# Kernel tuning notes

Measured on AMD Instinct MI355X. Metric: run time of the kernel, lower is better.

Reference implementation:

```python
import jax, jax.numpy as jnp
import numpy as np

N_HEADS = 16
ROPE_DIMS = 64


def _rope_tables(T, rd):
    # freqs: 1 / 10000^(arange(0, rd, 2)/rd), shape [rd//2]
    freqs = 1.0 / (10000.0 ** (np.arange(0, rd, 2, dtype=np.float32) / np.float32(rd)))
    ang = np.outer(np.arange(T, dtype=np.float32), freqs)  # [T, rd//2]
    return jnp.asarray(np.cos(ang)), jnp.asarray(np.sin(ang))


def _apply_rope(x, cos, sin, rd):
    # x: [B, H, T, D]; rotate-half style on first rd dims
    x_rope, x_pass = x[..., :rd], x[..., rd:]
    x1, x2 = x_rope[..., : rd // 2], x_rope[..., rd // 2 :]
    c = cos[None, None]  # [1,1,T,rd//2]
    s = sin[None, None]
    x_rot = jnp.concatenate([x1 * c - x2 * s, x2 * c + x1 * s], axis=-1)
    return jnp.concatenate([x_rot, x_pass], axis=-1)


def setup_inputs() -> dict:
    key = jax.random.key(0)
    k1, k2, k3 = jax.random.split(key, 3)
    B, T, C = 32, 512, 2048
    x = jax.random.normal(k1, (B, T, C), dtype=jnp.float32)
    w_qkv = jax.random.normal(k2, (3 * C, C), dtype=jnp.float32) * 0.02
    w_out = jax.random.normal(k3, (C, C), dtype=jnp.float32) * 0.02
    return {"x": x, "w_qkv": w_qkv, "w_out": w_out}


def reference(x, w_qkv, w_out):
    B, T, C = x.shape
    H = N_HEADS
    D = C // H
    # fused QKV projection: F.linear(x, w) = x @ w.T
    qkv = jnp.einsum('btc,fc->btf', x, w_qkv).reshape(B, T, 3, H, D)
    q = jnp.transpose(qkv[:, :, 0], (0, 2, 1, 3))  # [B,H,T,D]
    k = jnp.transpose(qkv[:, :, 1], (0, 2, 1, 3))
    v = jnp.transpose(qkv[:, :, 2], (0, 2, 1, 3))
    cos, sin = _rope_tables(T, ROPE_DIMS)
    q = _apply_rope(q, cos, sin, ROPE_DIMS)
    k = _apply_rope(k, cos, sin, ROPE_DIMS)
    # causal SDPA
    scale = 1.0 / jnp.sqrt(jnp.asarray(D, dtype=x.dtype))
    scores = jnp.einsum('bhqd,bhkd->bhqk', q, k) * scale
    causal = jnp.tril(jnp.ones((T, T), dtype=bool))
    scores = jnp.where(causal[None, None], scores, jnp.finfo(scores.dtype).min)
    attn = jax.nn.softmax(scores, axis=-1)
    y = jnp.einsum('bhqk,bhkd->bhqd', attn, v)
    y = jnp.transpose(y, (0, 2, 1, 3)).reshape(B, T, C)
    return jnp.einsum('btc,fc->btf', y, w_out)
```

## Files before the change

### kernel.cpp

```cpp
#include <hip/hip_runtime.h>


typedef __bf16 bf16x8 __attribute__((ext_vector_type(8)));
typedef float floatx4 __attribute__((ext_vector_type(4)));

__device__ __forceinline__ unsigned short f2bf(float f) {
  union { float f; unsigned u; } v; v.f = f;
  unsigned r = v.u + 0x7FFFu + ((v.u >> 16) & 1u);
  return (unsigned short)(r >> 16);
}
__device__ __forceinline__ float bf2f(unsigned short h) {
  union { unsigned u; float f; } v; v.u = ((unsigned)h) << 16; return v.f;
}

__device__ __forceinline__ void load_lds16(const void* g, void* l) {
  __builtin_amdgcn_global_load_lds((__attribute__((address_space(1))) void*)g,
                                   (__attribute__((address_space(3))) void*)l,
                                   16, 0, 0);
}

#define BARRIER() asm volatile("s_barrier" ::: "memory")
#define VMCNT6()  asm volatile("s_waitcnt vmcnt(6)" ::: "memory")
#define VMCNT0()  asm volatile("s_waitcnt vmcnt(0)" ::: "memory")

__global__ void rope_tables(float* __restrict__ cost, float* __restrict__ sint) {
  int i = blockIdx.x * 256 + threadIdx.x;
  if (i >= 512 * 32) return;
  int t = i >> 5, f = i & 31;
  float e = -(float)(2 * f) / 64.0f;
  float freq = powf(10000.0f, e);
  float ang = (float)t * freq;
  cost[i] = cosf(ang);
  sint[i] = sinf(ang);
}

__global__ void cast_bf16(const float* __restrict__ in,
                          unsigned short* __restrict__ out, int n8) {
  int i = blockIdx.x * 256 + threadIdx.x;
  if (i >= n8) return;
  float4 a = ((const float4*)in)[2 * i];
  float4 b = ((const float4*)in)[2 * i + 1];
  union { uint4 v; unsigned short u[8]; } o;
  o.u[0] = f2bf(a.x); o.u[1] = f2bf(a.y); o.u[2] = f2bf(a.z); o.u[3] = f2bf(a.w);
  o.u[4] = f2bf(b.x); o.u[5] = f2bf(b.y); o.u[6] = f2bf(b.z); o.u[7] = f2bf(b.w);
  ((uint4*)out)[i] = o.v;
}

__global__ __launch_bounds__(256) void rope_apply(
    unsigned short* __restrict__ qkv, const float* __restrict__ cost,
    const float* __restrict__ sint) {
  const int idx = blockIdx.x * 256 + threadIdx.x;
  const int tok = idx >> 4, h = idx & 15;
  const int t = tok & 511;
  const float scale = 0.08838834764831845f * 1.4426950408889634f;
  unsigned short* qrow = qkv + (size_t)tok * 6144 + h * 128;
  unsigned short* krow = qrow + 2048;

  float cs[32], sn[32];
#pragma unroll
  for (int j = 0; j < 8; ++j) {
    *(float4*)&cs[j * 4] = *(const float4*)&cost[t * 32 + j * 4];
    *(float4*)&sn[j * 4] = *(const float4*)&sint[t * 32 + j * 4];
  }
  union u32x4 { uint4 v[4]; unsigned short u[32]; };
  u32x4 q1, q2, k1, k2, o1, o2, o3, o4;
#pragma unroll
  for (int j = 0; j < 4; ++j) {
    q1.v[j] = *(const uint4*)(qrow + j * 8);
    q2.v[j] = *(const uint4*)(qrow + 32 + j * 8);
    k1.v[j] = *(const uint4*)(krow + j * 8);
    k2.v[j] = *(const uint4*)(krow + 32 + j * 8);
  }
#pragma unroll
  for (int d = 0; d < 32; ++d) {
    float c = cs[d], s = sn[d];
    float qx1 = bf2f(q1.u[d]), qx2 = bf2f(q2.u[d]);
    o1.u[d] = f2bf((qx1 * c - qx2 * s) * scale);
    o2.u[d] = f2bf((qx2 * c + qx1 * s) * scale);
    float kx1 = bf2f(k1.u[d]), kx2 = bf2f(k2.u[d]);
    o3.u[d] = f2bf(kx1 * c - kx2 * s);
    o4.u[d] = f2bf(kx2 * c + kx1 * s);
  }
#pragma unroll
  for (int j = 0; j < 4; ++j) {
    *(uint4*)(qrow + j * 8)      = o1.v[j];
    *(uint4*)(qrow + 32 + j * 8) = o2.v[j];
    *(uint4*)(krow + j * 8)      = o3.v[j];
    *(uint4*)(krow + 32 + j * 8) = o4.v[j];
  }
#pragma unroll
  for (int j = 0; j < 8; ++j) {
    union { uint4 v; unsigned short u[8]; } p, po;
    p.v = *(const uint4*)(qrow + 64 + j * 8);
#pragma unroll
    for (int jj = 0; jj < 8; ++jj) po.u[jj] = f2bf(bf2f(p.u[jj]) * scale);
    *(uint4*)(qrow + 64 + j * 8) = po.v;
  }
}

template <int OUT_BF16>
__global__ __launch_bounds__(512, 2) void gemm256(
    const unsigned short* __restrict__ A, const unsigned short* __restrict__ Bt,
    void* __restrict__ Cout, int M, int N, int K) {
  __shared__ __align__(16) unsigned short As[2][16384];
  __shared__ __align__(16) unsigned short Bs[2][16384];

  const int tid = threadIdx.x;
  const int nbx = gridDim.x;
  const int nwg = nbx * gridDim.y;
  const int lin = blockIdx.y * nbx + blockIdx.x;
  const int swz = (lin & 7) * (nwg >> 3) + (lin >> 3);
  const int bm = swz / nbx, bn = swz % nbx;

  const int w = tid >> 6, l = tid & 63;
  const int wm = w >> 2, wn = w & 3;
  const int quad = l >> 4, cl = l & 15;
  const int xs0 = ((0 + quad) ^ (cl & 7)) << 3;
  const int xs1 = ((4 + quad) ^ (cl & 7)) << 3;
  const int aoff = (wm * 128 + cl) * 64;
  const int boff = (wn * 64 + cl) * 64;

  const int srow = tid >> 3;
  const int lc = (tid & 7) ^ (srow & 7);
  const unsigned short* Ag = A + (size_t)(bm * 256 + srow) * K + lc * 8;
  const unsigned short* Bg = Bt + (size_t)(bn * 256 + srow) * K + lc * 8;

  auto stageA = [&](int q, int h, int k0) {
    const unsigned short* src = Ag + (size_t)(h * 128) * K + k0;
    unsigned short* dst = &As[q][0] + h * 8192 + tid * 8;
    load_lds16(src, dst);
    load_lds16(src + (size_t)64 * K, dst + 4096);
  };
  auto stageB = [&](int q, int h, int k0) {
    const unsigned short* src = Bg + (size_t)(h * 128) * K + k0;
    unsigned short* dst = &Bs[q][0] + h * 8192 + tid * 8;
    load_lds16(src, dst);
    load_lds16(src + (size_t)64 * K, dst + 4096);
  };

  floatx4 acc[8][4] = {};
  const int NT = K >> 6;

  stageA(0, 0, 0);  stageA(0, 1, 0);  stageB(0, 0, 0);  stageB(0, 1, 0);
  stageA(1, 0, 64); stageA(1, 1, 64); stageB(1, 0, 64);
  VMCNT6();
  BARRIER();

  for (int t = 0; t < NT; ++t) {
    const int q = t & 1;
    const unsigned short* pA = &As[q][0] + aoff;
    const unsigned short* pB = &Bs[q][0] + boff;
    const int k2 = (t + 2) << 6;
    const bool s2 = (t + 2) < NT;

    bf16x8 a0[4][2], a1[4][2], b0[2][2], b1[2][2];
#pragma unroll
    for (int mi = 0; mi < 4; ++mi) {
      a0[mi][0] = *(const bf16x8*)(pA + mi * 1024 + xs0);
      a0[mi][1] = *(const bf16x8*)(pA + mi * 1024 + xs1);
    }
#pragma unroll
    for (int ni = 0; ni < 2; ++ni) {
      b0[ni][0] = *(const bf16x8*)(pB + ni * 1024 + xs0);
      b0[ni][1] = *(const bf16x8*)(pB + ni * 1024 + xs1);
    }
    if (t + 1 < NT) stageB(q ^ 1, 1, (t + 1) << 6);
    BARRIER();
    __builtin_amdgcn_s_setprio(1);
#pragma unroll
    for (int mi = 0; mi < 4; ++mi)
#pragma unroll
      for (int ni = 0; ni < 2; ++ni)
#pragma unroll
        for (int ks = 0; ks < 2; ++ks)
          acc[mi][ni] = __builtin_amdgcn_mfma_f32_16x16x32_bf16(
              a0[mi][ks], b0[ni][ks], acc[mi][ni], 0, 0, 0);
    __builtin_amdgcn_s_setprio(0);
    BARRIER();
#pragma unroll
    for (int mi = 0; mi < 4; ++mi) {
      a1[mi][0] = *(const bf16x8*)(pA + (mi + 4) * 1024 + xs0);
      a1[mi][1] = *(const bf16x8*)(pA + (mi + 4) * 1024 + xs1);
    }
    BARRIER();
    __builtin_amdgcn_s_setprio(1);
#pragma unroll
    for (int mi = 0; mi < 4; ++mi)
#pragma unroll
      for (int ni = 0; ni < 2; ++ni)
#pragma unroll
        for (int ks = 0; ks < 2; ++ks)
          acc[mi + 4][ni] = __builtin_amdgcn_mfma_f32_16x16x32_bf16(
              a1[mi][ks], b0[ni][ks], acc[mi + 4][ni], 0, 0, 0);
    __builtin_amdgcn_s_setprio(0);
    BARRIER();
#pragma unroll
    for (int ni = 0; ni < 2; ++ni) {
      b1[ni][0] = *(const bf16x8*)(pB + (ni + 2) * 1024 + xs0);
      b1[ni][1] = *(const bf16x8*)(pB + (ni + 2) * 1024 + xs1);
    }
    if (s2) stageA(q, 0, k2);
    BARRIER();
    __builtin_amdgcn_s_setprio(1);
#pragma unroll
    for (int mi = 0; mi < 4; ++mi)
#pragma unroll
      for (int ni = 0; ni < 2; ++ni)
#pragma unroll
        for (int ks = 0; ks < 2; ++ks)
          acc[mi + 4][ni + 2] = __builtin_amdgcn_mfma_f32_16x16x32_bf16(
              a1[mi][ks], b1[ni][ks], acc[mi + 4][ni + 2], 0, 0, 0);
    __builtin_amdgcn_s_setprio(0);
    BARRIER();
    if (s2) { stageA(q, 1, k2); stageB(q, 0, k2); }
    BARRIER();
    __builtin_amdgcn_s_setprio(1);
#pragma unroll
    for (int mi = 0; mi < 4; ++mi)
#pragma unroll
      for (int ni = 0; ni < 2; ++ni)
#pragma unroll
        for (int ks = 0; ks < 2; ++ks)
          acc[mi][ni + 2] = __builtin_amdgcn_mfma_f32_16x16x32_bf16(
              a0[mi][ks], b1[ni][ks], acc[mi][ni + 2], 0, 0, 0);
    __builtin_amdgcn_s_setprio(0);
    if (t < NT - 2) { VMCNT6(); } else { VMCNT0(); }
    BARRIER();
  }

#pragma unroll
  for (int mi = 0; mi < 8; ++mi)
#pragma unroll
    for (int ni = 0; ni < 4; ++ni)
#pragma unroll
      for (int r = 0; r < 4; ++r) {
        const int gm = bm * 256 + wm * 128 + mi * 16 + quad * 4 + r;
        const int gn = bn * 256 + wn * 64 + ni * 16 + cl;
        const float v = acc[mi][ni][r];
        if (OUT_BF16)
          ((unsigned short*)Cout)[(size_t)gm * N + gn] = f2bf(v);
        else
          ((float*)Cout)[(size_t)gm * N + gn] = v;
      }
}

__global__ __launch_bounds__(256) void attn_kernel(
    const unsigned short* __restrict__ qkv, unsigned short* __restrict__ y) {
  __shared__ __align__(16) unsigned short Ks[2][64][128];
  __shared__ __align__(16) unsigned short VTs[2][128][64];
  __shared__ __align__(16) unsigned short Ps[4][16][72];

  const int bh = blockIdx.x, qt = blockIdx.y;
  const int b = bh >> 4, h = bh & 15;
  const int tid = threadIdx.x, w = tid >> 6, l = tid & 63;
  const int quad = l >> 4, cl = l & 15;

  bf16x8 aq[4];
  {
    const unsigned short* qrow =
        qkv + (size_t)(b * 512 + qt * 64 + w * 16 + cl) * 6144 + h * 128 +
        quad * 8;
#pragma unroll
    for (int kc = 0; kc < 4; ++kc) aq[kc] = *(const bf16x8*)(qrow + kc * 32);
  }

  const int krow = tid >> 4;
  const int kslot = tid & 15;
  const int kchunk = (kslot & 8) | ((kslot & 7) ^ (krow & 7));
  const unsigned short* kgbase =
      qkv + (size_t)(b * 512) * 6144 + 2048 + h * 128 + kchunk * 8;
  auto stageK = [&](int buf, int kt) {
#pragma unroll
    for (int slab = 0; slab < 4; ++slab) {
      const unsigned short* src =
          kgbase + (size_t)(kt * 64 + slab * 16 + krow) * 6144;
      load_lds16(src, &Ks[buf][0][0] + slab * 2048 + tid * 8);
    }
  };

  const int rowg = tid >> 5, colg = tid & 31;
  const unsigned short* vgbase =
      qkv + (size_t)(b * 512 + rowg * 8) * 6144 + 4096 + h * 128 + colg * 4;
  uint2 rv[8];
  auto loadV = [&](int kt) {
    const unsigned short* p = vgbase + (size_t)(kt * 64) * 6144;
#pragma unroll
    for (int rr = 0; rr < 8; ++rr) rv[rr] = *(const uint2*)(p + (size_t)rr * 6144);
  };
  auto writeV = [&](int buf) {
#pragma unroll
    for (int c = 0; c < 4; ++c) {
      const int d = colg * 4 + c;
      unsigned out[4];
#pragma unroll
      for (int p = 0; p < 4; ++p) {
        unsigned ua = ((const unsigned*)&rv[2 * p])[c >> 1];
        unsigned ub = ((const unsigned*)&rv[2 * p + 1])[c >> 1];
        unsigned lo = (c & 1) ? (ua >> 16) : (ua & 0xffffu);
        unsigned hi = (c & 1) ? (ub >> 16) : (ub & 0xffffu);
        out[p] = lo | (hi << 16);
      }
      *(uint4*)&VTs[buf][d][(rowg ^ (d & 7)) << 3] = *(uint4*)out;
    }
  };

  floatx4 o[8] = {};
  float m_i[4] = {-__builtin_inff(), -__builtin_inff(), -__builtin_inff(),
                  -__builtin_inff()};
  float l_i[4] = {0.f, 0.f, 0.f, 0.f};

  stageK(0, 0);
  loadV(0);
  VMCNT0();
  writeV(0);
  __syncthreads();

  for (int kt = 0; kt <= qt; ++kt) {
    const int qb = kt & 1;
    const bool more = (kt < qt);
    if (more) { stageK(qb ^ 1, kt + 1); loadV(kt + 1); }

    floatx4 s[4] = {};
    __builtin_amdgcn_s_setprio(1);
#pragma unroll
    for (int kc = 0; kc < 4; ++kc) {
#pragma unroll
      for (int nt = 0; nt < 4; ++nt) {
        const int row = nt * 16 + cl;
        const int c = kc * 4 + quad;
        const int sc = (c & 8) | ((c & 7) ^ (row & 7));
        bf16x8 bk = *(const bf16x8*)(&Ks[qb][row][sc * 8]);
        s[nt] = __builtin_amdgcn_mfma_f32_16x16x32_bf16(aq[kc], bk, s[nt], 0, 0, 0);
      }
    }
    __builtin_amdgcn_s_setprio(0);
    if (kt == qt) {
#pragma unroll
      for (int nt = 0; nt < 4; ++nt)
#pragma unroll
        for (int r = 0; r < 4; ++r) {
          int qrow_l = w * 16 + quad * 4 + r;
          int kcol_l = nt * 16 + cl;
          if (kcol_l > qrow_l) s[nt][r] = -__builtin_inff();
        }
    }
#pragma unroll
    for (int r = 0; r < 4; ++r) {
      float mx = fmaxf(fmaxf(s[0][r], s[1][r]), fmaxf(s[2][r], s[3][r]));
      mx = fmaxf(mx, __shfl_xor(mx, 1));
      mx = fmaxf(mx, __shfl_xor(mx, 2));
      mx = fmaxf(mx, __shfl_xor(mx, 4));
      mx = fmaxf(mx, __shfl_xor(mx, 8));
      float mn = fmaxf(m_i[r], mx);
      float a = exp2f(m_i[r] - mn);
      float rs = 0.f;
#pragma unroll
      for (int nt = 0; nt < 4; ++nt) {
        float p = exp2f(s[nt][r] - mn);
        s[nt][r] = p;
        rs += p;
      }
      rs += __shfl_xor(rs, 1);
      rs += __shfl_xor(rs, 2);
      rs += __shfl_xor(rs, 4);
      rs += __shfl_xor(rs, 8);
      l_i[r] = l_i[r] * a + rs;
      m_i[r] = mn;
#pragma unroll
      for (int nt2 = 0; nt2 < 8; ++nt2) o[nt2][r] *= a;
#pragma unroll
      for (int nt = 0; nt < 4; ++nt)
        Ps[w][quad * 4 + r][nt * 16 + cl] = f2bf(s[nt][r]);
    }

    __builtin_amdgcn_s_setprio(1);
#pragma unroll
    for (int kc2 = 0; kc2 < 2; ++kc2) {
      bf16x8 ap = *(const bf16x8*)(&Ps[w][cl][kc2 * 32 + quad * 8]);
#pragma unroll
      for (int nt2 = 0; nt2 < 8; ++nt2) {
        bf16x8 bv = *(const bf16x8*)(
            &VTs[qb][nt2 * 16 + cl][((kc2 * 4 + quad) ^ (cl & 7)) << 3]);
        o[nt2] = __builtin_amdgcn_mfma_f32_16x16x32_bf16(ap, bv, o[nt2], 0, 0, 0);
      }
    }
    __builtin_amdgcn_s_setprio(0);

    if (more) {
      VMCNT0();
      writeV(qb ^ 1);
    }
    __syncthreads();
  }

#pragma unroll
  for (int r = 0; r < 4; ++r) {
    float inv = 1.0f / l_i[r];
    size_t row =
        (size_t)(b * 512 + qt * 64 + w * 16 + quad * 4 + r) * 2048 + h * 128;
#pragma unroll
    for (int nt2 = 0; nt2 < 8; ++nt2)
      y[row + nt2 * 16 + cl] = f2bf(o[nt2][r] * inv);
  }
}

extern "C" void kernel_launch(void* const* d_in, const int* in_sizes, int n_in,
                              void* d_out, int out_size, void* d_ws,
                              size_t ws_size, hipStream_t stream) {
  const float* x = (const float*)d_in[0];
  const float* wqkv = (const float*)d_in[1];
  const float* wout = (const float*)d_in[2];
  float* out = (float*)d_out;

  char* ws = (char*)d_ws;
  float* cost = (float*)ws;            ws += (size_t)512 * 32 * 4;
  float* sint = (float*)ws;            ws += (size_t)512 * 32 * 4;
  unsigned short* xb = (unsigned short*)ws;    ws += (size_t)16384 * 2048 * 2;
  unsigned short* wqkvb = (unsigned short*)ws; ws += (size_t)6144 * 2048 * 2;
  unsigned short* woutb = (unsigned short*)ws; ws += (size_t)2048 * 2048 * 2;
  unsigned short* qkvb = (unsigned short*)ws;  ws += (size_t)16384 * 6144 * 2;
  unsigned short* yb = (unsigned short*)ws;    ws += (size_t)16384 * 2048 * 2;

  rope_tables<<<dim3(64), dim3(256), 0, stream>>>(cost, sint);
  cast_bf16<<<dim3(16384), dim3(256), 0, stream>>>(x, xb, 33554432 / 8);
  cast_bf16<<<dim3(6144), dim3(256), 0, stream>>>(wqkv, wqkvb, 12582912 / 8);
  cast_bf16<<<dim3(2048), dim3(256), 0, stream>>>(wout, woutb, 4194304 / 8);
  gemm256<1><<<dim3(24, 64), dim3(512), 0, stream>>>(xb, wqkvb, (void*)qkvb,
                                                     16384, 6144, 2048);
  rope_apply<<<dim3(1024), dim3(256), 0, stream>>>(qkvb, cost, sint);
  attn_kernel<<<dim3(512, 8), dim3(256), 0, stream>>>(qkvb, yb);
  gemm256<0><<<dim3(8, 64), dim3(512), 0, stream>>>(yb, woutb, (void*)out,
                                                    16384, 2048, 2048);
}
```

Measured before the change: 1.027 ms.

## Process 128 query rows per attention block with 8 waves and shared K/V tiles

```diff
diff --git a/kernel.cpp b/kernel.cpp
--- a/kernel.cpp
+++ b/kernel.cpp
@@ -244,63 +244,67 @@
       }
 }
 
-__global__ __launch_bounds__(256) void attn_kernel(
+__global__ __launch_bounds__(512, 4) void attn_kernel(
     const unsigned short* __restrict__ qkv, unsigned short* __restrict__ y) {
   __shared__ __align__(16) unsigned short Ks[2][64][128];
-  __shared__ __align__(16) unsigned short VTs[2][128][64];
-  __shared__ __align__(16) unsigned short Ps[4][16][72];
+  __shared__ __align__(16) unsigned short VTs[128][64];
+  __shared__ __align__(16) unsigned short Ps[8][16][72];
 
   const int bh = blockIdx.x, qt = blockIdx.y;
   const int b = bh >> 4, h = bh & 15;
   const int tid = threadIdx.x, w = tid >> 6, l = tid & 63;
   const int quad = l >> 4, cl = l & 15;
+  const int qbase = qt * 128 + w * 16;
 
   bf16x8 aq[4];
   {
     const unsigned short* qrow =
-        qkv + (size_t)(b * 512 + qt * 64 + w * 16 + cl) * 6144 + h * 128 +
-        quad * 8;
+        qkv + (size_t)(b * 512 + qbase + cl) * 6144 + h * 128 + quad * 8;
 #pragma unroll
     for (int kc = 0; kc < 4; ++kc) aq[kc] = *(const bf16x8*)(qrow + kc * 32);
   }
 
-  const int krow = tid >> 4;
-  const int kslot = tid & 15;
-  const int kchunk = (kslot & 8) | ((kslot & 7) ^ (krow & 7));
+  const int srow = tid >> 4;
+  const int slot = tid & 15;
+  const int kchunk = (slot & 8) | ((slot & 7) ^ (srow & 7));
   const unsigned short* kgbase =
       qkv + (size_t)(b * 512) * 6144 + 2048 + h * 128 + kchunk * 8;
   auto stageK = [&](int buf, int kt) {
 #pragma unroll
-    for (int slab = 0; slab < 4; ++slab) {
+    for (int slab = 0; slab < 2; ++slab) {
       const unsigned short* src =
-          kgbase + (size_t)(kt * 64 + slab * 16 + krow) * 6144;
-      load_lds16(src, &Ks[buf][0][0] + slab * 2048 + tid * 8);
+          kgbase + (size_t)(kt * 64 + slab * 32 + srow) * 6144;
+      load_lds16(src, &Ks[buf][0][0] + slab * 4096 + tid * 8);
     }
   };
 
-  const int rowg = tid >> 5, colg = tid & 31;
+  const int rowg = tid >> 5;
+  const int colg = tid & 31;
   const unsigned short* vgbase =
-      qkv + (size_t)(b * 512 + rowg * 8) * 6144 + 4096 + h * 128 + colg * 4;
-  uint2 rv[8];
+      qkv + (size_t)(b * 512 + rowg * 4) * 6144 + 4096 + h * 128 + colg * 4;
+  uint2 rv[4];
   auto loadV = [&](int kt) {
     const unsigned short* p = vgbase + (size_t)(kt * 64) * 6144;
 #pragma unroll
-    for (int rr = 0; rr < 8; ++rr) rv[rr] = *(const uint2*)(p + (size_t)rr * 6144);
+    for (int rr = 0; rr < 4; ++rr)
+      rv[rr] = *(const uint2*)(p + (size_t)rr * 6144);
   };
-  auto writeV = [&](int buf) {
+  auto writeV = [&]() {
 #pragma unroll
     for (int c = 0; c < 4; ++c) {
       const int d = colg * 4 + c;
-      unsigned out[4];
-#pragma unroll
-      for (int p = 0; p < 4; ++p) {
-        unsigned ua = ((const unsigned*)&rv[2 * p])[c >> 1];
-        unsigned ub = ((const unsigned*)&rv[2 * p + 1])[c >> 1];
-        unsigned lo = (c & 1) ? (ua >> 16) : (ua & 0xffffu);
-        unsigned hi = (c & 1) ? (ub >> 16) : (ub & 0xffffu);
-        out[p] = lo | (hi << 16);
-      }
-      *(uint4*)&VTs[buf][d][(rowg ^ (d & 7)) << 3] = *(uint4*)out;
+      unsigned a0 = ((const unsigned*)&rv[0])[c >> 1];
+      unsigned a1 = ((const unsigned*)&rv[1])[c >> 1];
+      unsigned a2 = ((const unsigned*)&rv[2])[c >> 1];
+      unsigned a3 = ((const unsigned*)&rv[3])[c >> 1];
+      unsigned l0 = (c & 1) ? (a0 >> 16) : (a0 & 0xffffu);
+      unsigned l1 = (c & 1) ? (a1 >> 16) : (a1 & 0xffffu);
+      unsigned l2 = (c & 1) ? (a2 >> 16) : (a2 & 0xffffu);
+      unsigned l3 = (c & 1) ? (a3 >> 16) : (a3 & 0xffffu);
+      uint2 val;
+      val.x = l0 | (l1 << 16);
+      val.y = l2 | (l3 << 16);
+      *(uint2*)&VTs[d][(((rowg >> 1) ^ (d & 7)) << 3) + (rowg & 1) * 4] = val;
     }
   };
 
@@ -309,95 +313,102 @@
                   -__builtin_inff()};
   float l_i[4] = {0.f, 0.f, 0.f, 0.f};
 
+  const int KT = 2 * qt + 2;
+
   stageK(0, 0);
   loadV(0);
-  VMCNT0();
-  writeV(0);
   __syncthreads();
-
-  for (int kt = 0; kt <= qt; ++kt) {
+  writeV();
+  __syncthreads();
+
+  for (int kt = 0; kt < KT; ++kt) {
     const int qb = kt & 1;
-    const bool more = (kt < qt);
+    const bool more = (kt + 1 < KT);
     if (more) { stageK(qb ^ 1, kt + 1); loadV(kt + 1); }
 
-    floatx4 s[4] = {};
-    __builtin_amdgcn_s_setprio(1);
-#pragma unroll
-    for (int kc = 0; kc < 4; ++kc) {
-#pragma unroll
-      for (int nt = 0; nt < 4; ++nt) {
-        const int row = nt * 16 + cl;
-        const int c = kc * 4 + quad;
-        const int sc = (c & 8) | ((c & 7) ^ (row & 7));
-        bf16x8 bk = *(const bf16x8*)(&Ks[qb][row][sc * 8]);
-        s[nt] = __builtin_amdgcn_mfma_f32_16x16x32_bf16(aq[kc], bk, s[nt], 0, 0, 0);
+    const bool active = (kt * 64 <= qbase);
+    if (active) {
+      floatx4 s[4] = {};
+      __builtin_amdgcn_s_setprio(1);
+#pragma unroll
+      for (int kc = 0; kc < 4; ++kc) {
+#pragma unroll
+        for (int nt = 0; nt < 4; ++nt) {
+          const int row = nt * 16 + cl;
+          const int c = kc * 4 + quad;
+          const int sc = (c & 8) | ((c & 7) ^ (row & 7));
+          bf16x8 bk = *(const bf16x8*)(&Ks[qb][row][sc * 8]);
+          s[nt] =
+              __builtin_amdgcn_mfma_f32_16x16x32_bf16(aq[kc], bk, s[nt], 0, 0, 0);
+        }
       }
-    }
-    __builtin_amdgcn_s_setprio(0);
-    if (kt == qt) {
-#pragma unroll
-      for (int nt = 0; nt < 4; ++nt)
-#pragma unroll
-        for (int r = 0; r < 4; ++r) {
-          int qrow_l = w * 16 + quad * 4 + r;
-          int kcol_l = nt * 16 + cl;
-          if (kcol_l > qrow_l) s[nt][r] = -__builtin_inff();
+      __builtin_amdgcn_s_setprio(0);
+      if (qbase < kt * 64 + 64) {
+#pragma unroll
+        for (int nt = 0; nt < 4; ++nt)
+#pragma unroll
+          for (int r = 0; r < 4; ++r) {
+            int qrow_g = qbase + quad * 4 + r;
+            int kcol_g = kt * 64 + nt * 16 + cl;
+            if (kcol_g > qrow_g) s[nt][r] = -__builtin_inff();
+          }
+      }
+#pragma unroll
+      for (int r = 0; r < 4; ++r) {
+        float mx = fmaxf(fmaxf(s[0][r], s[1][r]), fmaxf(s[2][r], s[3][r]));
+        mx = fmaxf(mx, __shfl_xor(mx, 1));
+        mx = fmaxf(mx, __shfl_xor(mx, 2));
+        mx = fmaxf(mx, __shfl_xor(mx, 4));
+        mx = fmaxf(mx, __shfl_xor(mx, 8));
+        float mn = fmaxf(m_i[r], mx);
+        float a = exp2f(m_i[r] - mn);
+        float rs = 0.f;
+#pragma unroll
+        for (int nt = 0; nt < 4; ++nt) {
+          float p = exp2f(s[nt][r] - mn);
+          s[nt][r] = p;
+          rs += p;
         }
-    }
-#pragma unroll
-    for (int r = 0; r < 4; ++r) {
-      float mx = fmaxf(fmaxf(s[0][r], s[1][r]), fmaxf(s[2][r], s[3][r]));
-      mx = fmaxf(mx, __shfl_xor(mx, 1));
-      mx = fmaxf(mx, __shfl_xor(mx, 2));
-      mx = fmaxf(mx, __shfl_xor(mx, 4));
-      mx = fmaxf(mx, __shfl_xor(mx, 8));
-      float mn = fmaxf(m_i[r], mx);
-      float a = exp2f(m_i[r] - mn);
-      float rs = 0.f;
-#pragma unroll
-      for (int nt = 0; nt < 4; ++nt) {
-        float p = exp2f(s[nt][r] - mn);
-        s[nt][r] = p;
-        rs += p;
+        rs += __shfl_xor(rs, 1);
+        rs += __shfl_xor(rs, 2);
+        rs += __shfl_xor(rs, 4);
+        rs += __shfl_xor(rs, 8);
+        l_i[r] = l_i[r] * a + rs;
+        m_i[r] = mn;
+#pragma unroll
+        for (int nt2 = 0; nt2 < 8; ++nt2) o[nt2][r] *= a;
+#pragma unroll
+        for (int nt = 0; nt < 4; ++nt)
+          Ps[w][quad * 4 + r][nt * 16 + cl] = f2bf(s[nt][r]);
       }
-      rs += __shfl_xor(rs, 1);
-      rs += __shfl_xor(rs, 2);
-      rs += __shfl_xor(rs, 4);
-      rs += __shfl_xor(rs, 8);
-      l_i[r] = l_i[r] * a + rs;
-      m_i[r] = mn;
-#pragma unroll
-      for (int nt2 = 0; nt2 < 8; ++nt2) o[nt2][r] *= a;
-#pragma unroll
-      for (int nt = 0; nt < 4; ++nt)
-        Ps[w][quad * 4 + r][nt * 16 + cl] = f2bf(s[nt][r]);
-    }
-
-    __builtin_amdgcn_s_setprio(1);
-#pragma unroll
-    for (int kc2 = 0; kc2 < 2; ++kc2) {
-      bf16x8 ap = *(const bf16x8*)(&Ps[w][cl][kc2 * 32 + quad * 8]);
-#pragma unroll
-      for (int nt2 = 0; nt2 < 8; ++nt2) {
-        bf16x8 bv = *(const bf16x8*)(
-            &VTs[qb][nt2 * 16 + cl][((kc2 * 4 + quad) ^ (cl & 7)) << 3]);
-        o[nt2] = __builtin_amdgcn_mfma_f32_16x16x32_bf16(ap, bv, o[nt2], 0, 0, 0);
+
+      __builtin_amdgcn_s_setprio(1);
+#pragma unroll
+      for (int kc2 = 0; kc2 < 2; ++kc2) {
+        bf16x8 ap = *(const bf16x8*)(&Ps[w][cl][kc2 * 32 + quad * 8]);
+#pragma unroll
+        for (int nt2 = 0; nt2 < 8; ++nt2) {
+          bf16x8 bv = *(const bf16x8*)(
+              &VTs[nt2 * 16 + cl][((kc2 * 4 + quad) ^ (cl & 7)) << 3]);
+          o[nt2] =
+              __builtin_amdgcn_mfma_f32_16x16x32_bf16(ap, bv, o[nt2], 0, 0, 0);
+        }
       }
-    }
-    __builtin_amdgcn_s_setprio(0);
+      __builtin_amdgcn_s_setprio(0);
+    }
 
     if (more) {
-      VMCNT0();
-      writeV(qb ^ 1);
-    }
-    __syncthreads();
+      __syncthreads();
+      writeV();
+      __syncthreads();
+    }
   }
 
 #pragma unroll
   for (int r = 0; r < 4; ++r) {
     float inv = 1.0f / l_i[r];
     size_t row =
-        (size_t)(b * 512 + qt * 64 + w * 16 + quad * 4 + r) * 2048 + h * 128;
+        (size_t)(b * 512 + qbase + quad * 4 + r) * 2048 + h * 128;
 #pragma unroll
     for (int nt2 = 0; nt2 < 8; ++nt2)
       y[row + nt2 * 16 + cl] = f2bf(o[nt2][r] * inv);
@@ -428,7 +439,7 @@
   gemm256<1><<<dim3(24, 64), dim3(512), 0, stream>>>(xb, wqkvb, (void*)qkvb,
                                                      16384, 6144, 2048);
   rope_apply<<<dim3(1024), dim3(256), 0, stream>>>(qkvb, cost, sint);
-  attn_kernel<<<dim3(512, 8), dim3(256), 0, stream>>>(qkvb, yb);
+  attn_kernel<<<dim3(512, 4), dim3(512), 0, stream>>>(qkvb, yb);
   gemm256<0><<<dim3(8, 64), dim3(512), 0, stream>>>(yb, woutb, (void*)out,
                                                     16384, 2048, 2048);
 }
```

Result: faster. 986.2 us (-4.0%).
